# Performance work log

Hardware: AMD Instinct MI355X
Metric: run time of the kernel (lower is better)

## Reference

```python
import jax, jax.numpy as jnp
import numpy as np

T = 12   # num orientations (target fiber)
S = 12   # num orientations (source fiber)
ATTR = 3
IN = 32
OUT = 32
B = 400000


def setup_inputs() -> dict:
    key = jax.random.key(0)
    k1, k2, k3 = jax.random.split(key, 3)
    x = jax.random.normal(k1, (B, S, IN), dtype=jnp.float32)
    edge_attr_fiber = jax.random.normal(k2, (T, S, ATTR), dtype=jnp.float32)
    # Linear(attr_dim, out_dim*in_dim, bias=False): weight [out*in, attr]
    W = jax.random.normal(k3, (OUT * IN, ATTR), dtype=jnp.float32) * (1.0 / np.sqrt(ATTR))
    b = jnp.zeros((OUT,), dtype=jnp.float32)
    return {"x": x, "edge_attr_fiber": edge_attr_fiber, "W": W, "b": b}


def reference(x, edge_attr_fiber, W, b):
    # kernel_fiber = Linear(edge_attr_fiber): [t,s,attr] @ [attr, out*in] -> [t,s,out*in]
    kernel = jnp.einsum('tsa,ka->tsk', edge_attr_fiber, W)
    kernel = kernel.reshape(T, S, OUT, IN)  # [t,s,o,i]
    out = jnp.einsum('tsoi,bsi->bto', kernel, x)
    return out + b
```

## Files before the change

kernel.cpp:

```cpp
#include <hip/hip_runtime.h>


using f32x4  = __attribute__((ext_vector_type(4))) float;
using bf16x8 = __attribute__((ext_vector_type(8))) __bf16;
using short8 = __attribute__((ext_vector_type(8))) short;

constexpr int T_   = 12;
constexpr int S_   = 12;
constexpr int ATTR = 3;
constexpr int IN   = 32;
constexpr int OUT  = 32;
constexpr int K    = S_ * IN;
constexpr int N    = T_ * OUT;
constexpr int NB   = 400000;
constexpr int KB_CNT = K / 32;
constexpr int CT_CNT = N / 16;
constexpr int FRAG_SHORTS = 64 * 8;
constexpr int CT_SHORTS   = KB_CNT * FRAG_SHORTS;

__device__ __forceinline__ unsigned short f2bf(float f) {
  unsigned u = __builtin_bit_cast(unsigned, f);
  u += 0x7fffu + ((u >> 16) & 1u);
  return (unsigned short)(u >> 16);
}

__global__ __launch_bounds__(384) void build_B(const float* __restrict__ edge,
                                               const float* __restrict__ W,
                                               unsigned short* __restrict__ Bm) {
  const int n = blockIdx.x;
  const int k = threadIdx.x;
  const int t = n >> 5, o = n & 31;
  const int s = k >> 5, i = k & 31;
  const float* e = edge + (t * S_ + s) * ATTR;
  const float* w = W + (o * IN + i) * ATTR;
  const float v = e[0] * w[0] + e[1] * w[1] + e[2] * w[2];
  const int ct = n >> 4, l15 = n & 15;
  const int kb = k >> 5, quad = (k >> 3) & 3, j = k & 7;
  const int lane = (quad << 4) | l15;
  Bm[((ct * KB_CNT + kb) * 64 + lane) * 8 + j] = f2bf(v);
}

__device__ __forceinline__ void stage_B(const unsigned short* __restrict__ Bm, int ct,
                                        unsigned short* dst, int wid, int lane) {
  const unsigned short* src = Bm + (size_t)ct * CT_SHORTS;
#pragma unroll
  for (int q = 0; q < 3; ++q) {
    const int c = wid * 3 + q;
    __builtin_amdgcn_global_load_lds(
        (const __attribute__((address_space(1))) void*)(src + c * FRAG_SHORTS + lane * 8),
        (__attribute__((address_space(3))) void*)(dst + c * FRAG_SHORTS),
        16, 0, 0);
  }
}

__global__ __launch_bounds__(256, 2) void fiber_gemm(
    const float* __restrict__ x, const unsigned short* __restrict__ Bm,
    const float* __restrict__ bias, float* __restrict__ out) {
  __shared__ __align__(16) unsigned short Bl[2][CT_SHORTS];

  const int lane = threadIdx.x & 63;
  const int wid  = threadIdx.x >> 6;
  const int col  = lane & 15;
  const int quad = lane >> 4;
  const int rowbase = blockIdx.x * 128 + wid * 32;

  stage_B(Bm, 0, &Bl[0][0], wid, lane);
  __builtin_amdgcn_sched_barrier(0);

  bf16x8 Xf[2][KB_CNT];
#pragma unroll
  for (int mt = 0; mt < 2; ++mt) {
    const float* xp = x + (size_t)(rowbase + mt * 16 + col) * K + quad * 8;
#pragma unroll
    for (int kb = 0; kb < KB_CNT; ++kb) {
      const f32x4 lo = *(const f32x4*)(xp + kb * 32);
      const f32x4 hi = *(const f32x4*)(xp + kb * 32 + 4);
      short8 sv;
#pragma unroll
      for (int j = 0; j < 4; ++j) {
        sv[j]     = (short)f2bf(lo[j]);
        sv[j + 4] = (short)f2bf(hi[j]);
      }
      Xf[mt][kb] = __builtin_bit_cast(bf16x8, sv);
    }
  }

  f32x4 bv0, bv1;
#pragma unroll
  for (int r = 0; r < 4; ++r) {
    bv0[r] = bias[quad * 4 + r];
    bv1[r] = bias[16 + quad * 4 + r];
  }

  asm volatile("s_waitcnt vmcnt(0)" ::: "memory");
  __builtin_amdgcn_s_barrier();

#pragma unroll 1
  for (int ct = 0; ct < CT_CNT; ++ct) {
    const int cur = ct & 1;
    if (ct + 1 < CT_CNT) {
      stage_B(Bm, ct + 1, &Bl[cur ^ 1][0], wid, lane);
      __builtin_amdgcn_sched_barrier(0);
    }

    f32x4 acc0 = {0.f, 0.f, 0.f, 0.f};
    f32x4 acc1 = {0.f, 0.f, 0.f, 0.f};
    const unsigned short* bp = &Bl[cur][lane * 8];
#pragma unroll
    for (int kb = 0; kb < KB_CNT; ++kb) {
      const bf16x8 Bf = *(const bf16x8*)(bp + kb * FRAG_SHORTS);
      acc0 = __builtin_amdgcn_mfma_f32_16x16x32_bf16(Bf, Xf[0][kb], acc0, 0, 0, 0);
      acc1 = __builtin_amdgcn_mfma_f32_16x16x32_bf16(Bf, Xf[1][kb], acc1, 0, 0, 0);
    }

    const f32x4 bv = cur ? bv1 : bv0;
    float* op0 = out + (size_t)(rowbase + col) * N + ct * 16 + quad * 4;
    *(f32x4*)op0            = acc0 + bv;
    *(f32x4*)(op0 + 16 * N) = acc1 + bv;

    if (ct + 1 < CT_CNT) {
      asm volatile("s_waitcnt vmcnt(2)" ::: "memory");
      __builtin_amdgcn_s_barrier();
    }
  }
}

extern "C" void kernel_launch(void* const* d_in, const int* in_sizes, int n_in,
                              void* d_out, int out_size, void* d_ws, size_t ws_size,
                              hipStream_t stream) {
  const float* x    = (const float*)d_in[0];
  const float* edge = (const float*)d_in[1];
  const float* W    = (const float*)d_in[2];
  const float* bias = (const float*)d_in[3];
  float* out = (float*)d_out;
  unsigned short* Bm = (unsigned short*)d_ws;

  build_B<<<dim3(N), dim3(K), 0, stream>>>(edge, W, Bm);
  fiber_gemm<<<dim3(NB / 128), dim3(256), 0, stream>>>(x, Bm, bias, out);
}
```

Baseline: 1.040 ms.

## Read B fragments directly from global memory and use nontemporal x/out accesses

Drops the double-buffered LDS staging of B and the per-tile block barriers. Each wave now loads its B fragments straight from global memory, where they are small and L2-resident. Loads of x and stores of out become nontemporal so the streaming data does not pollute the caches. Launch bounds rise to 3 blocks per SM to raise occupancy, at the cost of redundant per-wave global/L2 reads of B and some register pressure.

```diff
diff --git a/kernel.cpp b/kernel.cpp
--- a/kernel.cpp
+++ b/kernel.cpp
@@ -40,32 +40,14 @@
   Bm[((ct * KB_CNT + kb) * 64 + lane) * 8 + j] = f2bf(v);
 }
 
-__device__ __forceinline__ void stage_B(const unsigned short* __restrict__ Bm, int ct,
-                                        unsigned short* dst, int wid, int lane) {
-  const unsigned short* src = Bm + (size_t)ct * CT_SHORTS;
-#pragma unroll
-  for (int q = 0; q < 3; ++q) {
-    const int c = wid * 3 + q;
-    __builtin_amdgcn_global_load_lds(
-        (const __attribute__((address_space(1))) void*)(src + c * FRAG_SHORTS + lane * 8),
-        (__attribute__((address_space(3))) void*)(dst + c * FRAG_SHORTS),
-        16, 0, 0);
-  }
-}
-
-__global__ __launch_bounds__(256, 2) void fiber_gemm(
+__global__ __launch_bounds__(256, 3) void fiber_gemm(
     const float* __restrict__ x, const unsigned short* __restrict__ Bm,
     const float* __restrict__ bias, float* __restrict__ out) {
-  __shared__ __align__(16) unsigned short Bl[2][CT_SHORTS];
-
   const int lane = threadIdx.x & 63;
   const int wid  = threadIdx.x >> 6;
   const int col  = lane & 15;
   const int quad = lane >> 4;
   const int rowbase = blockIdx.x * 128 + wid * 32;
-
-  stage_B(Bm, 0, &Bl[0][0], wid, lane);
-  __builtin_amdgcn_sched_barrier(0);
 
   bf16x8 Xf[2][KB_CNT];
 #pragma unroll
@@ -73,8 +55,8 @@
     const float* xp = x + (size_t)(rowbase + mt * 16 + col) * K + quad * 8;
 #pragma unroll
     for (int kb = 0; kb < KB_CNT; ++kb) {
-      const f32x4 lo = *(const f32x4*)(xp + kb * 32);
-      const f32x4 hi = *(const f32x4*)(xp + kb * 32 + 4);
+      const f32x4 lo = __builtin_nontemporal_load((const f32x4*)(xp + kb * 32));
+      const f32x4 hi = __builtin_nontemporal_load((const f32x4*)(xp + kb * 32 + 4));
       short8 sv;
 #pragma unroll
       for (int j = 0; j < 4; ++j) {
@@ -92,20 +74,11 @@
     bv1[r] = bias[16 + quad * 4 + r];
   }
 
-  asm volatile("s_waitcnt vmcnt(0)" ::: "memory");
-  __builtin_amdgcn_s_barrier();
-
 #pragma unroll 1
   for (int ct = 0; ct < CT_CNT; ++ct) {
-    const int cur = ct & 1;
-    if (ct + 1 < CT_CNT) {
-      stage_B(Bm, ct + 1, &Bl[cur ^ 1][0], wid, lane);
-      __builtin_amdgcn_sched_barrier(0);
-    }
-
+    const unsigned short* bp = Bm + (size_t)ct * CT_SHORTS + lane * 8;
     f32x4 acc0 = {0.f, 0.f, 0.f, 0.f};
     f32x4 acc1 = {0.f, 0.f, 0.f, 0.f};
-    const unsigned short* bp = &Bl[cur][lane * 8];
 #pragma unroll
     for (int kb = 0; kb < KB_CNT; ++kb) {
       const bf16x8 Bf = *(const bf16x8*)(bp + kb * FRAG_SHORTS);
@@ -113,15 +86,9 @@
       acc1 = __builtin_amdgcn_mfma_f32_16x16x32_bf16(Bf, Xf[1][kb], acc1, 0, 0, 0);
     }
 
-    const f32x4 bv = cur ? bv1 : bv0;
     float* op0 = out + (size_t)(rowbase + col) * N + ct * 16 + quad * 4;
-    *(f32x4*)op0            = acc0 + bv;
-    *(f32x4*)(op0 + 16 * N) = acc1 + bv;
-
-    if (ct + 1 < CT_CNT) {
-      asm volatile("s_waitcnt vmcnt(2)" ::: "memory");
-      __builtin_amdgcn_s_barrier();
-    }
+    __builtin_nontemporal_store(acc0 + (ct & 1 ? bv1 : bv0), (f32x4*)op0);
+    __builtin_nontemporal_store(acc1 + (ct & 1 ? bv1 : bv0), (f32x4*)(op0 + 16 * N));
   }
 }
 
```

New measurement: 1.166 ms. +12.1%, slower.
